# Optimization experiments

Measured on AMD Instinct MI355X. Metric: run time of the kernel, lower is better.

## Reference

```python
import jax, jax.numpy as jnp
import numpy as np

B, S, D, H = 2, 2048, 1024, 16
HD = D // H  # head dim = 64


def setup_inputs() -> dict:
    key = jax.random.key(0)
    ks = jax.random.split(key, 5)
    scale = 0.02
    x = jax.random.normal(ks[0], (B, S, D), dtype=jnp.float32)
    Wqkv = jax.random.normal(ks[1], (D, 3 * D), dtype=jnp.float32) * scale
    bqkv = jnp.zeros((3 * D,), dtype=jnp.float32)
    Wproj = jax.random.normal(ks[2], (D, D), dtype=jnp.float32) * scale
    bproj = jnp.zeros((D,), dtype=jnp.float32)
    return {"x": x, "Wqkv": Wqkv, "bqkv": bqkv, "Wproj": Wproj, "bproj": bproj}


def reference(x, Wqkv, bqkv, Wproj, bproj):
    # fused QKV projection
    qkv = x @ Wqkv + bqkv                      # [B, S, 3D]
    q, k, v = jnp.split(qkv, 3, axis=-1)       # each [B, S, D]
    # split heads -> [B, H, S, HD]
    def heads(t):
        return t.reshape(B, S, H, HD).transpose(0, 2, 1, 3)
    q, k, v = heads(q), heads(k), heads(v)
    # scaled dot-product attention with causal mask (GPT-2 style)
    scores = jnp.einsum('bhqd,bhkd->bhqk', q, k) / jnp.sqrt(jnp.float32(HD))
    causal = jnp.tril(jnp.ones((S, S), dtype=bool))
    scores = jnp.where(causal, scores, jnp.finfo(scores.dtype).min)
    attn = jax.nn.softmax(scores, axis=-1)      # [B, H, S, S]
    out = jnp.einsum('bhqk,bhkd->bhqd', attn, v)  # [B, H, S, HD]
    out = out.transpose(0, 2, 1, 3).reshape(B, S, D)
    return out @ Wproj + bproj
```

## Files before the change

kernel.cpp:

```cpp
#include <hip/hip_runtime.h>
#include <hip/hip_bf16.h>


typedef __attribute__((ext_vector_type(8))) short short8;
typedef __attribute__((ext_vector_type(4))) float float4v;

#define S_LEN 2048
#define NHEAD 16
#define HDIM  64
#define DMODEL 1024

__device__ __forceinline__ unsigned short f2bf(float f) {
    union { float f; unsigned u; } v; v.f = f;
    unsigned r = v.u + 0x7FFF + ((v.u >> 16) & 1);
    return (unsigned short)(r >> 16);
}

__device__ __forceinline__ unsigned fbits_rn(float f) {
    union { float f; unsigned u; } v; v.f = f;
    return v.u + 0x8000u;
}

__device__ __forceinline__ void async16(const void* g, const void* l) {
    __builtin_amdgcn_global_load_lds(
        (const __attribute__((address_space(1))) unsigned int*)g,
        (__attribute__((address_space(3))) unsigned int*)l, 16, 0, 0);
}

__global__ void f32_to_bf16_v4(const float4* __restrict__ in,
                               ushort4* __restrict__ out, int n4) {
    int i = blockIdx.x * blockDim.x + threadIdx.x;
    if (i < n4) {
        float4 v = in[i];
        ushort4 o;
        o.x = f2bf(v.x); o.y = f2bf(v.y); o.z = f2bf(v.z); o.w = f2bf(v.w);
        out[i] = o;
    }
}

__global__ __launch_bounds__(256) void w_transpose_bf16(
    const float* __restrict__ Wqkv, const float* __restrict__ Wproj,
    unsigned short* __restrict__ outQ, unsigned short* __restrict__ outP) {
    __shared__ float t[64][65];
    const float* in; unsigned short* out; int N, bxl;
    if (blockIdx.x < 48) { in = Wqkv;  out = outQ; N = 3072; bxl = blockIdx.x; }
    else                 { in = Wproj; out = outP; N = 1024; bxl = blockIdx.x - 48; }
    const int K = 1024;
    const int kb = blockIdx.y * 64, nb = bxl * 64;
    const int tid = threadIdx.x;
    const int r0 = tid >> 4, c0 = (tid & 15) * 4;
#pragma unroll
    for (int g = 0; g < 4; g++) {
        float4 v = *(const float4*)(in + (size_t)(kb + g * 16 + r0) * N + nb + c0);
        t[g * 16 + r0][c0 + 0] = v.x; t[g * 16 + r0][c0 + 1] = v.y;
        t[g * 16 + r0][c0 + 2] = v.z; t[g * 16 + r0][c0 + 3] = v.w;
    }
    __syncthreads();
#pragma unroll
    for (int g = 0; g < 4; g++) {
        int n = g * 16 + r0;
        ushort4 o;
        o.x = f2bf(t[c0 + 0][n]); o.y = f2bf(t[c0 + 1][n]);
        o.z = f2bf(t[c0 + 2][n]); o.w = f2bf(t[c0 + 3][n]);
        *(ushort4*)(out + (size_t)(nb + n) * K + kb + c0) = o;
    }
}

#define QSCALE 0.18033688f

__global__ __launch_bounds__(256) void gemm_qkv_kernel(
    const unsigned short* __restrict__ A,
    const unsigned short* __restrict__ Bt,
    const float* __restrict__ bias,
    unsigned short* __restrict__ out_q,
    unsigned short* __restrict__ out_kp,
    unsigned short* __restrict__ out_vp,
    int M, int N, int K)
{
    __shared__ unsigned short smem[128 * 132];
    unsigned short* As = smem;
    unsigned short* Bs = smem + 8192;

    const int tid  = threadIdx.x;
    const int lane = tid & 63;
    const int wave = tid >> 6;
    const int quad = lane >> 4;
    const int l16  = lane & 15;

    const int m0 = blockIdx.y * 128;
    const int n0 = blockIdx.x * 128;
    const int wm = (wave >> 1) * 64;
    const int wn = (wave & 1) * 64;

    float4v acc[4][4];
#pragma unroll
    for (int i = 0; i < 4; i++)
#pragma unroll
        for (int j = 0; j < 4; j++) acc[i][j] = (float4v){0.f, 0.f, 0.f, 0.f};

    const int srow = lane >> 2;
    const int scol = (lane & 3) * 8;

    for (int k0 = 0; k0 < K; k0 += 64) {
        __syncthreads();
#pragma unroll
        for (int kk = 0; kk < 2; kk++)
#pragma unroll
            for (int it = 0; it < 2; it++) {
                const int rg = it * 64 + wave * 16;
                async16(A  + (size_t)(m0 + rg + srow) * K + k0 + kk * 32 + scol,
                        (const char*)(As + kk * 4096) + rg * 64);
                async16(Bt + (size_t)(n0 + rg + srow) * K + k0 + kk * 32 + scol,
                        (const char*)(Bs + kk * 4096) + rg * 64);
            }
        __syncthreads();

#pragma unroll
        for (int kk = 0; kk < 2; kk++) {
            short8 af[4], bf[4];
#pragma unroll
            for (int mt = 0; mt < 4; mt++)
                af[mt] = *(const short8*)(As + kk * 4096
                                          + (wm + mt * 16 + l16) * 32 + quad * 8);
#pragma unroll
            for (int nt = 0; nt < 4; nt++)
                bf[nt] = *(const short8*)(Bs + kk * 4096
                                          + (wn + nt * 16 + l16) * 32 + quad * 8);
#pragma unroll
            for (int mt = 0; mt < 4; mt++)
#pragma unroll
                for (int nt = 0; nt < 4; nt++)
                    acc[mt][nt] = __builtin_amdgcn_mfma_f32_16x16x32_bf16(
                        af[mt], bf[nt], acc[mt][nt], 0, 0, 0);
        }
    }

    __syncthreads();
#pragma unroll
    for (int nt = 0; nt < 4; nt++) {
        const int col = n0 + wn + nt * 16 + l16;
        const float sc = ((col >> 10) == 0) ? QSCALE : 1.0f;
        const float bia = bias[col] * sc;
        const int cold = (wn + nt * 16 + l16) >> 1;
#pragma unroll
        for (int mt = 0; mt < 4; mt++)
#pragma unroll
            for (int r = 0; r < 4; r++) {
                unsigned fb = fbits_rn(acc[mt][nt][r] * sc + bia);
                unsigned fbp = (unsigned)__shfl_xor((int)fb, 1, 64);
                unsigned pd = (l16 & 1)
                    ? __builtin_amdgcn_perm(fb, fbp, 0x07060302)
                    : __builtin_amdgcn_perm(fbp, fb, 0x07060302);
                const int rowl = wm + mt * 16 + quad * 4 + r;
                *((unsigned*)smem + rowl * 66 + cold) = pd;
            }
    }
    __syncthreads();

#pragma unroll
    for (int ps = 0; ps < 8; ps++) {
        const int row = ps * 16 + (tid >> 4);
        const int pc  = tid & 15;
        const int col0 = pc * 8;
        const int cb = n0 + (col0 >> 6) * 64;
        const int part = cb >> 10;
        const int hh = (cb & 1023) >> 6;
        const int gr = m0 + row;
        const int b = gr >> 11, s = gr & 2047;
        const size_t bhI = (size_t)(b * NHEAD + hh);
        if (part == 2) {
            const int l2  = tid >> 4;
            const int q2  = pc & 3;
            const int kk2 = (pc >> 2) & 1;
            const int nt2 = ps & 3;
            const int colb = (pc >> 3) * 64 + nt2 * 16 + l2;
            const int rowb = (ps >> 2) * 64;
            union { unsigned short u[8]; uint4 q; } wv;
#pragma unroll
            for (int j = 0; j < 8; j++) {
                const int key = (kk2 * 2 + (j >> 2)) * 16 + q2 * 4 + (j & 3);
                wv.u[j] = smem[(rowb + key) * 132 + colb];
            }
            unsigned short* po = out_vp
                + ((((bhI * 32 + (s >> 6)) * 4 + nt2) * 2 + kk2) * 64
                   + q2 * 16 + l2) * 8;
            *(uint4*)po = wv.q;
        } else {
            const unsigned short* pl = smem + row * 132 + col0;
            uint2 a = *(const uint2*)(pl);
            uint2 bb = *(const uint2*)(pl + 4);
            uint4 w; w.x = a.x; w.y = a.y; w.z = bb.x; w.w = bb.y;
            unsigned short* po;
            if (part == 1) {
                const int hd = col0 & 63;
                const int h = hd >> 5, q = (hd >> 3) & 3;
                po = out_kp + ((((bhI * 32 + (s >> 6)) * 4 + ((s >> 4) & 3)) * 2
                                + h) * 64 + q * 16 + (s & 15)) * 8;
            } else {
                po = out_q + (bhI * S_LEN + s) * HDIM + (col0 & 63);
            }
            *(uint4*)po = w;
        }
    }
}

__global__ __launch_bounds__(256) void gemm_proj_kernel(
    const unsigned short* __restrict__ A,
    const unsigned short* __restrict__ Bt,
    const float* __restrict__ bias,
    float* __restrict__ out_f,
    int M, int N, int K)
{
    __shared__ unsigned short smem[12288];
    unsigned short* As = smem;
    unsigned short* Bs = smem + 4096;

    const int tid  = threadIdx.x;
    const int lane = tid & 63;
    const int wave = tid >> 6;
    const int quad = lane >> 4;
    const int l16  = lane & 15;

    const int m0 = blockIdx.y * 64;
    const int n0 = blockIdx.x * 128;
    const int wm = (wave >> 1) * 32;
    const int wn = (wave & 1) * 64;

    float4v acc[2][4];
#pragma unroll
    for (int i = 0; i < 2; i++)
#pragma unroll
        for (int j = 0; j < 4; j++) acc[i][j] = (float4v){0.f, 0.f, 0.f, 0.f};

    const int srow = lane >> 2;
    const int scol = (lane & 3) * 8;

    for (int k0 = 0; k0 < K; k0 += 64) {
        __syncthreads();
#pragma unroll
        for (int kk = 0; kk < 2; kk++) {
            async16(A + (size_t)(m0 + wave * 16 + srow) * K + k0 + kk * 32 + scol,
                    (const char*)(As + kk * 2048) + wave * 1024);
#pragma unroll
            for (int it = 0; it < 2; it++) {
                const int rg = it * 64 + wave * 16;
                async16(Bt + (size_t)(n0 + rg + srow) * K + k0 + kk * 32 + scol,
                        (const char*)(Bs + kk * 4096) + rg * 64);
            }
        }
        __syncthreads();

#pragma unroll
        for (int kk = 0; kk < 2; kk++) {
            short8 af[2], bf[4];
#pragma unroll
            for (int mt = 0; mt < 2; mt++)
                af[mt] = *(const short8*)(As + kk * 2048
                                          + (wm + mt * 16 + l16) * 32 + quad * 8);
#pragma unroll
            for (int nt = 0; nt < 4; nt++)
                bf[nt] = *(const short8*)(Bs + kk * 4096
                                          + (wn + nt * 16 + l16) * 32 + quad * 8);
#pragma unroll
            for (int mt = 0; mt < 2; mt++)
#pragma unroll
                for (int nt = 0; nt < 4; nt++)
                    acc[mt][nt] = __builtin_amdgcn_mfma_f32_16x16x32_bf16(
                        af[mt], bf[nt], acc[mt][nt], 0, 0, 0);
        }
    }

#pragma unroll
    for (int nt = 0; nt < 4; nt++) {
        const int col = n0 + wn + nt * 16 + l16;
        const float bia = bias[col];
#pragma unroll
        for (int mt = 0; mt < 2; mt++) {
            const int rowb = m0 + wm + mt * 16 + quad * 4;
#pragma unroll
            for (int r = 0; r < 4; r++)
                out_f[(size_t)(rowb + r) * N + col] = acc[mt][nt][r] + bia;
        }
    }
}

__global__ __launch_bounds__(256) void attn6p_kernel(
    const unsigned short* __restrict__ Q,
    const unsigned short* __restrict__ Kp,
    const unsigned short* __restrict__ Vp,
    unsigned short* __restrict__ ctx)
{
    __shared__ unsigned short lds[3][8192];

    const int tid  = threadIdx.x;
    const int lane = tid & 63;
    const int wave = tid >> 6;
    const int quad = lane >> 4;
    const int l16  = lane & 15;

    const int bx = blockIdx.x;
    const int bh = bx & 31;
    const int qb = 31 - (bx >> 5);
    const int q0 = qb * 64 + wave * 16;
    const int nch = qb + 1;

    const size_t baseQ = (size_t)bh * S_LEN * HDIM;
    const unsigned short* kb_ = Kp + (size_t)bh * 32 * 4096;
    const unsigned short* vb_ = Vp + (size_t)bh * 32 * 4096;

    short8 qf[2];
#pragma unroll
    for (int h = 0; h < 2; h++)
        qf[h] = *(const short8*)(Q + baseQ + (size_t)(q0 + l16) * HDIM
                                 + h * 32 + quad * 8);

    float4v o[4];
#pragma unroll
    for (int nt = 0; nt < 4; nt++) o[nt] = (float4v){0.f, 0.f, 0.f, 0.f};
    float lsa[4] = {0.f, 0.f, 0.f, 0.f};

    {
        unsigned short* sb = &lds[0][0];
        async16(kb_ + tid * 8,        sb + wave * 512);
        async16(kb_ + 2048 + tid * 8, sb + 2048 + wave * 512);
        async16(vb_ + tid * 8,        sb + 4096 + wave * 512);
        async16(vb_ + 2048 + tid * 8, sb + 6144 + wave * 512);
    }
    if (nch > 1) {
        const unsigned short* kc = kb_ + 4096;
        const unsigned short* vc = vb_ + 4096;
        unsigned short* sb = &lds[1][0];
        async16(kc + tid * 8,        sb + wave * 512);
        async16(kc + 2048 + tid * 8, sb + 2048 + wave * 512);
        async16(vc + tid * 8,        sb + 4096 + wave * 512);
        async16(vc + 2048 + tid * 8, sb + 6144 + wave * 512);
    }

    int rb = 0;
    for (int c = 0; c < nch; c++) {
        if (c + 1 < nch) asm volatile("s_waitcnt vmcnt(4)" ::: "memory");
        else             asm volatile("s_waitcnt vmcnt(0)" ::: "memory");
        __builtin_amdgcn_s_barrier();
        __builtin_amdgcn_sched_barrier(0);

        const unsigned short* lb = &lds[rb][0];

        short8 kf[4][2];
#pragma unroll
        for (int kt = 0; kt < 4; kt++)
#pragma unroll
            for (int h = 0; h < 2; h++)
                kf[kt][h] = *(const short8*)(lb + ((kt * 2 + h) * 64 + lane) * 8);

        if (c + 2 < nch) {
            const int sbi = (rb + 2 >= 3) ? rb - 1 : rb + 2;
            const unsigned short* kc = kb_ + (size_t)(c + 2) * 4096;
            const unsigned short* vc = vb_ + (size_t)(c + 2) * 4096;
            unsigned short* sb = &lds[sbi][0];
            async16(kc + tid * 8,        sb + wave * 512);
            async16(kc + 2048 + tid * 8, sb + 2048 + wave * 512);
            async16(vc + tid * 8,        sb + 4096 + wave * 512);
            async16(vc + 2048 + tid * 8, sb + 6144 + wave * 512);
        }

        float4v st[4];
#pragma unroll
        for (int kt = 0; kt < 4; kt++) {
            st[kt] = __builtin_amdgcn_mfma_f32_16x16x32_bf16(
                kf[kt][0], qf[0], (float4v){0.f, 0.f, 0.f, 0.f}, 0, 0, 0);
            st[kt] = __builtin_amdgcn_mfma_f32_16x16x32_bf16(
                kf[kt][1], qf[1], st[kt], 0, 0, 0);
        }

        short8 vf[4][2];
#pragma unroll
        for (int nt = 0; nt < 4; nt++)
#pragma unroll
            for (int kk = 0; kk < 2; kk++)
                vf[nt][kk] = *(const short8*)(lb + 4096
                                              + ((nt * 2 + kk) * 64 + lane) * 8);

        const bool lastc = (c == nch - 1);
        const int kb0 = c * 64;
        const int qpos = q0 + l16;
        float p[4][4];
#pragma unroll
        for (int kt = 0; kt < 4; kt++)
#pragma unroll
            for (int r = 0; r < 4; r++) {
                float x = st[kt][r];
                if (lastc) {
                    int kpos = kb0 + kt * 16 + quad * 4 + r;
                    x = (kpos <= qpos) ? x : -1e30f;
                }
                p[kt][r] = __builtin_amdgcn_exp2f(x);
                lsa[kt] += p[kt][r];
            }

        unsigned pk[4][2];
#pragma unroll
        for (int kt = 0; kt < 4; kt++)
#pragma unroll
            for (int j = 0; j < 2; j++)
                pk[kt][j] = __builtin_amdgcn_perm(
                    fbits_rn(p[kt][2 * j + 1]), fbits_rn(p[kt][2 * j]),
                    0x07060302);
        union { unsigned u[4]; short8 s; } pf[2];
#pragma unroll
        for (int kk = 0; kk < 2; kk++)
#pragma unroll
            for (int pp = 0; pp < 4; pp++)
                pf[kk].u[pp] = pk[kk * 2 + (pp >> 1)][pp & 1];

#pragma unroll
        for (int nt = 0; nt < 4; nt++) {
            o[nt] = __builtin_amdgcn_mfma_f32_16x16x32_bf16(
                pf[0].s, vf[nt][0], o[nt], 0, 0, 0);
            o[nt] = __builtin_amdgcn_mfma_f32_16x16x32_bf16(
                pf[1].s, vf[nt][1], o[nt], 0, 0, 0);
        }

        rb = (rb + 1 == 3) ? 0 : rb + 1;
    }

    float l = (lsa[0] + lsa[1]) + (lsa[2] + lsa[3]);
    l += __shfl_xor(l, 16, 64);
    l += __shfl_xor(l, 32, 64);
    const float linv = 1.f / l;
    float lr[4];
#pragma unroll
    for (int r = 0; r < 4; r++) lr[r] = __shfl(linv, quad * 4 + r, 64);

    const int b = bh >> 4, h = bh & 15;
#pragma unroll
    for (int r = 0; r < 4; r++) {
        const int s = q0 + quad * 4 + r;
        const size_t off = ((size_t)(b * S_LEN + s)) * DMODEL + h * HDIM;
#pragma unroll
        for (int nt = 0; nt < 4; nt++)
            ctx[off + nt * 16 + l16] = f2bf(o[nt][r] * lr[r]);
    }
}

extern "C" void kernel_launch(void* const* d_in, const int* in_sizes, int n_in,
                              void* d_out, int out_size, void* d_ws, size_t ws_size,
                              hipStream_t stream) {
    const float* x     = (const float*)d_in[0];
    const float* Wqkv  = (const float*)d_in[1];
    const float* bqkv  = (const float*)d_in[2];
    const float* Wproj = (const float*)d_in[3];
    const float* bproj = (const float*)d_in[4];
    float* out = (float*)d_out;

    const int M  = 2 * S_LEN;
    const int N1 = 3 * DMODEL;
    const int K  = DMODEL;

    unsigned short* x_bf    = (unsigned short*)d_ws;
    unsigned short* wqkv_t  = x_bf   + (size_t)M * K;
    unsigned short* wproj_t = wqkv_t + (size_t)K * N1;
    unsigned short* q_bf    = wproj_t + (size_t)K * DMODEL;
    unsigned short* kp_bf   = q_bf   + (size_t)M * DMODEL;
    unsigned short* vp_bf   = kp_bf  + (size_t)M * DMODEL;
    unsigned short* ctx_bf  = vp_bf  + (size_t)M * DMODEL;

    {
        int n4 = (M * K) / 4;
        f32_to_bf16_v4<<<n4 / 256, 256, 0, stream>>>((const float4*)x,
                                                     (ushort4*)x_bf, n4);
    }
    {
        dim3 g(64, 16);
        w_transpose_bf16<<<g, 256, 0, stream>>>(Wqkv, Wproj, wqkv_t, wproj_t);
    }

    dim3 g1(N1 / 128, M / 128);
    gemm_qkv_kernel<<<g1, 256, 0, stream>>>(x_bf, wqkv_t, bqkv,
                                            q_bf, kp_bf, vp_bf, M, N1, K);

    attn6p_kernel<<<1024, 256, 0, stream>>>(q_bf, kp_bf, vp_bf, ctx_bf);

    dim3 g3(DMODEL / 128, M / 64);
    gemm_proj_kernel<<<g3, 256, 0, stream>>>(ctx_bf, wproj_t, bproj, out,
                                             M, DMODEL, K);
}
```

Measured before the change: 168.7 us.

## Double-buffer LDS tiles in QKV and projection GEMMs to overlap loads with MFMA

```diff
diff --git a/kernel.cpp b/kernel.cpp
--- a/kernel.cpp
+++ b/kernel.cpp
@@ -78,8 +78,6 @@
     int M, int N, int K)
 {
     __shared__ unsigned short smem[128 * 132];
-    unsigned short* As = smem;
-    unsigned short* Bs = smem + 8192;
 
     const int tid  = threadIdx.x;
     const int lane = tid & 63;
@@ -98,44 +96,56 @@
 #pragma unroll
         for (int j = 0; j < 4; j++) acc[i][j] = (float4v){0.f, 0.f, 0.f, 0.f};
 
-    const int srow = lane >> 2;
-    const int scol = (lane & 3) * 8;
-
-    for (int k0 = 0; k0 < K; k0 += 64) {
+    {
+        unsigned short* Ab = smem;
+        unsigned short* Bb = smem + 8192;
+#pragma unroll
+        for (int rd = 0; rd < 2; rd++) {
+            const int p = rd * 256 + tid;
+            async16(A  + (size_t)(m0 + (p >> 2)) * K + (p & 3) * 8,
+                    (const char*)Ab + p * 16);
+            async16(Bt + (size_t)(n0 + (p >> 2)) * K + (p & 3) * 8,
+                    (const char*)Bb + p * 16);
+        }
+    }
+    __syncthreads();
+
+    const int NT = 32;
+    for (int t = 0; t < NT; t++) {
+        const int cur = t & 1;
+        if (t + 1 < NT) {
+            const int k1 = (t + 1) * 32;
+            unsigned short* Ab = smem + (cur ^ 1) * 4096;
+            unsigned short* Bb = smem + 8192 + (cur ^ 1) * 4096;
+#pragma unroll
+            for (int rd = 0; rd < 2; rd++) {
+                const int p = rd * 256 + tid;
+                async16(A  + (size_t)(m0 + (p >> 2)) * K + k1 + (p & 3) * 8,
+                        (const char*)Ab + p * 16);
+                async16(Bt + (size_t)(n0 + (p >> 2)) * K + k1 + (p & 3) * 8,
+                        (const char*)Bb + p * 16);
+            }
+        }
+
+        const unsigned short* Ar = smem + cur * 4096;
+        const unsigned short* Br = smem + 8192 + cur * 4096;
+        short8 af[4], bf[4];
+#pragma unroll
+        for (int mt = 0; mt < 4; mt++)
+            af[mt] = *(const short8*)(Ar + (wm + mt * 16 + l16) * 32 + quad * 8);
+#pragma unroll
+        for (int nt = 0; nt < 4; nt++)
+            bf[nt] = *(const short8*)(Br + (wn + nt * 16 + l16) * 32 + quad * 8);
+#pragma unroll
+        for (int mt = 0; mt < 4; mt++)
+#pragma unroll
+            for (int nt = 0; nt < 4; nt++)
+                acc[mt][nt] = __builtin_amdgcn_mfma_f32_16x16x32_bf16(
+                    af[mt], bf[nt], acc[mt][nt], 0, 0, 0);
+
         __syncthreads();
-#pragma unroll
-        for (int kk = 0; kk < 2; kk++)
-#pragma unroll
-            for (int it = 0; it < 2; it++) {
-                const int rg = it * 64 + wave * 16;
-                async16(A  + (size_t)(m0 + rg + srow) * K + k0 + kk * 32 + scol,
-                        (const char*)(As + kk * 4096) + rg * 64);
-                async16(Bt + (size_t)(n0 + rg + srow) * K + k0 + kk * 32 + scol,
-                        (const char*)(Bs + kk * 4096) + rg * 64);
-            }
-        __syncthreads();
-
-#pragma unroll
-        for (int kk = 0; kk < 2; kk++) {
-            short8 af[4], bf[4];
-#pragma unroll
-            for (int mt = 0; mt < 4; mt++)
-                af[mt] = *(const short8*)(As + kk * 4096
-                                          + (wm + mt * 16 + l16) * 32 + quad * 8);
-#pragma unroll
-            for (int nt = 0; nt < 4; nt++)
-                bf[nt] = *(const short8*)(Bs + kk * 4096
-                                          + (wn + nt * 16 + l16) * 32 + quad * 8);
-#pragma unroll
-            for (int mt = 0; mt < 4; mt++)
-#pragma unroll
-                for (int nt = 0; nt < 4; nt++)
-                    acc[mt][nt] = __builtin_amdgcn_mfma_f32_16x16x32_bf16(
-                        af[mt], bf[nt], acc[mt][nt], 0, 0, 0);
-        }
-    }
-
-    __syncthreads();
+    }
+
 #pragma unroll
     for (int nt = 0; nt < 4; nt++) {
         const int col = n0 + wn + nt * 16 + l16;
@@ -212,8 +222,6 @@
     int M, int N, int K)
 {
     __shared__ unsigned short smem[12288];
-    unsigned short* As = smem;
-    unsigned short* Bs = smem + 4096;
 
     const int tid  = threadIdx.x;
     const int lane = tid & 63;
@@ -232,42 +240,54 @@
 #pragma unroll
         for (int j = 0; j < 4; j++) acc[i][j] = (float4v){0.f, 0.f, 0.f, 0.f};
 
-    const int srow = lane >> 2;
-    const int scol = (lane & 3) * 8;
-
-    for (int k0 = 0; k0 < K; k0 += 64) {
+    {
+        unsigned short* Ab = smem;
+        unsigned short* Bb = smem + 4096;
+        async16(A + (size_t)(m0 + (tid >> 2)) * K + (tid & 3) * 8,
+                (const char*)Ab + tid * 16);
+#pragma unroll
+        for (int rd = 0; rd < 2; rd++) {
+            const int p = rd * 256 + tid;
+            async16(Bt + (size_t)(n0 + (p >> 2)) * K + (p & 3) * 8,
+                    (const char*)Bb + p * 16);
+        }
+    }
+    __syncthreads();
+
+    const int NT = 32;
+    for (int t = 0; t < NT; t++) {
+        const int cur = t & 1;
+        if (t + 1 < NT) {
+            const int k1 = (t + 1) * 32;
+            unsigned short* Ab = smem + (cur ^ 1) * 2048;
+            unsigned short* Bb = smem + 4096 + (cur ^ 1) * 4096;
+            async16(A + (size_t)(m0 + (tid >> 2)) * K + k1 + (tid & 3) * 8,
+                    (const char*)Ab + tid * 16);
+#pragma unroll
+            for (int rd = 0; rd < 2; rd++) {
+                const int p = rd * 256 + tid;
+                async16(Bt + (size_t)(n0 + (p >> 2)) * K + k1 + (p & 3) * 8,
+                        (const char*)Bb + p * 16);
+            }
+        }
+
+        const unsigned short* Ar = smem + cur * 2048;
+        const unsigned short* Br = smem + 4096 + cur * 4096;
+        short8 af[2], bf[4];
+#pragma unroll
+        for (int mt = 0; mt < 2; mt++)
+            af[mt] = *(const short8*)(Ar + (wm + mt * 16 + l16) * 32 + quad * 8);
+#pragma unroll
+        for (int nt = 0; nt < 4; nt++)
+            bf[nt] = *(const short8*)(Br + (wn + nt * 16 + l16) * 32 + quad * 8);
+#pragma unroll
+        for (int mt = 0; mt < 2; mt++)
+#pragma unroll
+            for (int nt = 0; nt < 4; nt++)
+                acc[mt][nt] = __builtin_amdgcn_mfma_f32_16x16x32_bf16(
+                    af[mt], bf[nt], acc[mt][nt], 0, 0, 0);
+
         __syncthreads();
-#pragma unroll
-        for (int kk = 0; kk < 2; kk++) {
-            async16(A + (size_t)(m0 + wave * 16 + srow) * K + k0 + kk * 32 + scol,
-                    (const char*)(As + kk * 2048) + wave * 1024);
-#pragma unroll
-            for (int it = 0; it < 2; it++) {
-                const int rg = it * 64 + wave * 16;
-                async16(Bt + (size_t)(n0 + rg + srow) * K + k0 + kk * 32 + scol,
-                        (const char*)(Bs + kk * 4096) + rg * 64);
-            }
-        }
-        __syncthreads();
-
-#pragma unroll
-        for (int kk = 0; kk < 2; kk++) {
-            short8 af[2], bf[4];
-#pragma unroll
-            for (int mt = 0; mt < 2; mt++)
-                af[mt] = *(const short8*)(As + kk * 2048
-                                          + (wm + mt * 16 + l16) * 32 + quad * 8);
-#pragma unroll
-            for (int nt = 0; nt < 4; nt++)
-                bf[nt] = *(const short8*)(Bs + kk * 4096
-                                          + (wn + nt * 16 + l16) * 32 + quad * 8);
-#pragma unroll
-            for (int mt = 0; mt < 2; mt++)
-#pragma unroll
-                for (int nt = 0; nt < 4; nt++)
-                    acc[mt][nt] = __builtin_amdgcn_mfma_f32_16x16x32_bf16(
-                        af[mt], bf[nt], acc[mt][nt], 0, 0, 0);
-        }
     }
 
 #pragma unroll
```

New measurement: 171.3 us. Within noise of the previous version (+1.5%).

## Triple-buffer QKV GEMM LDS tiles with async prefetch two stages ahead

Applied to the files above, without the earlier changes.

```diff
diff --git a/kernel.cpp b/kernel.cpp
--- a/kernel.cpp
+++ b/kernel.cpp
@@ -77,9 +77,7 @@
     unsigned short* __restrict__ out_vp,
     int M, int N, int K)
 {
-    __shared__ unsigned short smem[128 * 132];
-    unsigned short* As = smem;
-    unsigned short* Bs = smem + 8192;
+    __shared__ unsigned short smem[24576];
 
     const int tid  = threadIdx.x;
     const int lane = tid & 63;
@@ -98,42 +96,56 @@
 #pragma unroll
         for (int j = 0; j < 4; j++) acc[i][j] = (float4v){0.f, 0.f, 0.f, 0.f};
 
-    const int srow = lane >> 2;
-    const int scol = (lane & 3) * 8;
-
-    for (int k0 = 0; k0 < K; k0 += 64) {
-        __syncthreads();
-#pragma unroll
-        for (int kk = 0; kk < 2; kk++)
-#pragma unroll
-            for (int it = 0; it < 2; it++) {
-                const int rg = it * 64 + wave * 16;
-                async16(A  + (size_t)(m0 + rg + srow) * K + k0 + kk * 32 + scol,
-                        (const char*)(As + kk * 4096) + rg * 64);
-                async16(Bt + (size_t)(n0 + rg + srow) * K + k0 + kk * 32 + scol,
-                        (const char*)(Bs + kk * 4096) + rg * 64);
-            }
-        __syncthreads();
-
-#pragma unroll
-        for (int kk = 0; kk < 2; kk++) {
-            short8 af[4], bf[4];
-#pragma unroll
-            for (int mt = 0; mt < 4; mt++)
-                af[mt] = *(const short8*)(As + kk * 4096
-                                          + (wm + mt * 16 + l16) * 32 + quad * 8);
+    const int NT = 32;
+#define QKV_STAGE(tt, bufi)                                                   \
+    {                                                                         \
+        const int k1 = (tt) * 32;                                             \
+        unsigned short* Ab = smem + (bufi) * 4096;                            \
+        unsigned short* Bb = smem + 12288 + (bufi) * 4096;                    \
+        _Pragma("unroll")                                                     \
+        for (int rd = 0; rd < 2; rd++) {                                      \
+            const int p = rd * 256 + tid;                                     \
+            async16(A  + (size_t)(m0 + (p >> 2)) * K + k1 + (p & 3) * 8,      \
+                    (const char*)Ab + p * 16);                                \
+            async16(Bt + (size_t)(n0 + (p >> 2)) * K + k1 + (p & 3) * 8,      \
+                    (const char*)Bb + p * 16);                                \
+        }                                                                     \
+    }
+
+    QKV_STAGE(0, 0);
+    QKV_STAGE(1, 1);
+
+    int rb = 0;
+    for (int t = 0; t < NT; t++) {
+        if (t + 1 < NT) asm volatile("s_waitcnt vmcnt(4)" ::: "memory");
+        else            asm volatile("s_waitcnt vmcnt(0)" ::: "memory");
+        __builtin_amdgcn_s_barrier();
+        __builtin_amdgcn_sched_barrier(0);
+
+        if (t + 2 < NT) {
+            const int sbi = (rb + 2 >= 3) ? rb - 1 : rb + 2;
+            QKV_STAGE(t + 2, sbi);
+        }
+
+        const unsigned short* Ar = smem + rb * 4096;
+        const unsigned short* Br = smem + 12288 + rb * 4096;
+        short8 af[4], bf[4];
+#pragma unroll
+        for (int mt = 0; mt < 4; mt++)
+            af[mt] = *(const short8*)(Ar + (wm + mt * 16 + l16) * 32 + quad * 8);
+#pragma unroll
+        for (int nt = 0; nt < 4; nt++)
+            bf[nt] = *(const short8*)(Br + (wn + nt * 16 + l16) * 32 + quad * 8);
+#pragma unroll
+        for (int mt = 0; mt < 4; mt++)
 #pragma unroll
             for (int nt = 0; nt < 4; nt++)
-                bf[nt] = *(const short8*)(Bs + kk * 4096
-                                          + (wn + nt * 16 + l16) * 32 + quad * 8);
-#pragma unroll
-            for (int mt = 0; mt < 4; mt++)
-#pragma unroll
-                for (int nt = 0; nt < 4; nt++)
-                    acc[mt][nt] = __builtin_amdgcn_mfma_f32_16x16x32_bf16(
-                        af[mt], bf[nt], acc[mt][nt], 0, 0, 0);
-        }
-    }
+                acc[mt][nt] = __builtin_amdgcn_mfma_f32_16x16x32_bf16(
+                    af[mt], bf[nt], acc[mt][nt], 0, 0, 0);
+
+        rb = (rb + 1 == 3) ? 0 : rb + 1;
+    }
+#undef QKV_STAGE
 
     __syncthreads();
 #pragma unroll
```

Result: no change. 167.9 us (-0.5%).
